# Optimization experiments

Measured on AMD Instinct MI355X. Metric: run time of the kernel, lower is better.

Reference implementation:

```python
import jax, jax.numpy as jnp
import numpy as np

B, C, H, W = 8, 256, 96, 96
GH, GW = 16, 16                # proto_grid
KH, KW = H // GH, W // GW      # avg-pool kernel = stride
P = GH * GW                    # local prototypes per sample
THRESH = 0.95
NORM_EPS = 1e-4


def _safe_norm(x, axis):
    # L2-normalize with norm clamped below at NORM_EPS (matches safe_norm)
    n = jnp.sqrt(jnp.sum(x * x, axis=axis, keepdims=True))
    return x / jnp.maximum(n, NORM_EPS)


def _avg_pool(x):
    # [B, c, H, W] -> [B, c, P] non-overlapping KHxKW average pooling
    b, c = x.shape[:2]
    return x.reshape(b, c, GH, KH, GW, KW).mean(axis=(3, 5)).reshape(b, c, P)


def setup_inputs() -> dict:
    key = jax.random.key(0)
    k1, k2, k3, k4 = jax.random.split(key, 4)
    qry_fts = jax.random.normal(k1, (B, C, H, W), dtype=jnp.float32)
    sup_fts = jax.random.normal(k2, (B, C, H, W), dtype=jnp.float32)
    sup_mask = (jax.random.uniform(k3, (B, 1, H, W)) > 0.02).astype(jnp.float32)
    true_bg_mask = (jax.random.uniform(k4, (B, 1, H, W)) > 0.9).astype(jnp.float32)
    return {"qry_fts": qry_fts, "sup_fts": sup_fts,
            "sup_mask": sup_mask, "true_bg_mask": true_bg_mask}


def reference(qry_fts, sup_fts, sup_mask, true_bg_mask):
    # mode='gridconv+' path, vectorized: ragged prototype selection -> masked softmax
    local_fts = _avg_pool(sup_fts).transpose(0, 2, 1)       # [B, P, C]
    local_mask = _avg_pool(sup_mask)[:, 0, :]               # [B, P]
    local_bg = _avg_pool(true_bg_mask)[:, 0, :]             # [B, P]
    valid = (local_mask > THRESH) & (local_bg < 0.5)        # [B, P] bool

    # global masked-average prototype
    gproto = jnp.sum(sup_fts * sup_mask, axis=(-1, -2)) / (
        jnp.sum(sup_mask, axis=(-1, -2)) + 1e-5)            # [B, C]

    protos = jnp.concatenate([local_fts, gproto[:, None, :]], axis=1)  # [B, P+1, C]
    valid_all = jnp.concatenate(
        [valid, jnp.ones((B, 1), dtype=bool)], axis=1)      # global always valid

    protos_n = _safe_norm(protos, axis=2)                   # [B, P+1, C]
    qry_n = _safe_norm(qry_fts, axis=1)                     # [B, C, H, W]

    # 1x1 conv with prototype weights == batched cosine similarity
    dists = jnp.einsum('bchw,bpc->bphw', qry_n, protos_n)   # [B, P+1, H, W]

    # softmax restricted to valid prototypes (invalid get weight 0)
    logits = jnp.where(valid_all[:, :, None, None], dists, -jnp.inf)
    w = jax.nn.softmax(logits, axis=1)
    pred = jnp.sum(w * dists, axis=1, keepdims=True)        # [B, 1, H, W]
    return pred
```

## Files before the change

kernel.cpp:

```cpp
#include <hip/hip_runtime.h>

#define BB 8
#define CC 256
#define HH 96
#define WW 96
#define HWW (HH*WW)
#define NLOC 256
#define PPAD 257
#define THRESH 0.95f
#define NORM_EPS 1e-4f

typedef __attribute__((ext_vector_type(8))) _Float16 f16x8;
typedef __attribute__((ext_vector_type(16))) float f32x16;

union H16 { _Float16 f; unsigned short u; };

__global__ void k01(const float* __restrict__ sup_fts,
                    const float* __restrict__ sup_mask,
                    const float* __restrict__ true_bg,
                    float* __restrict__ protos,
                    float* __restrict__ validf,
                    float* __restrict__ masksum) {
    __shared__ float red[256];
    int blk = blockIdx.x;
    int t = threadIdx.x;
    if (blk < BB * CC) {
        int b = blk >> 8, c = blk & 255;
        int gy = t >> 4, gx = t & 15;
        const float* fb = sup_fts + ((size_t)b * CC + c) * HWW;
        const float* mb = sup_mask + (size_t)b * HWW;
        int base = gy * 6 * WW + gx * 6;
        float fs = 0.f, fm = 0.f;
        for (int r = 0; r < 6; ++r) {
            const float* rowf = fb + base + r * WW;
            const float* rowm = mb + base + r * WW;
#pragma unroll
            for (int h = 0; h < 3; ++h) {
                float2 v  = *(const float2*)(rowf + 2 * h);
                float2 mk = *(const float2*)(rowm + 2 * h);
                fs += v.x + v.y;
                fm = fmaf(v.x, mk.x, fm);
                fm = fmaf(v.y, mk.y, fm);
            }
        }
        protos[((size_t)b * PPAD + t) * CC + c] = fs * (1.f / 36.f);
        red[t] = fm;
        __syncthreads();
        for (int off = 128; off > 0; off >>= 1) {
            if (t < off) red[t] += red[t + off];
            __syncthreads();
        }
        if (t == 0) protos[((size_t)b * PPAD + 256) * CC + c] = red[0];
    } else {
        int b = blk - BB * CC;
        int gy = t >> 4, gx = t & 15;
        const float* mb = sup_mask + (size_t)b * HWW;
        const float* gb = true_bg  + (size_t)b * HWW;
        int base = gy * 6 * WW + gx * 6;
        float ms = 0.f, bs = 0.f;
        for (int r = 0; r < 6; ++r) {
            const float* rowm = mb + base + r * WW;
            const float* rowg = gb + base + r * WW;
#pragma unroll
            for (int h = 0; h < 3; ++h) {
                float2 mk = *(const float2*)(rowm + 2 * h);
                float2 bg2 = *(const float2*)(rowg + 2 * h);
                ms += mk.x + mk.y;
                bs += bg2.x + bg2.y;
            }
        }
        float mmean = ms * (1.f / 36.f);
        float bmean = bs * (1.f / 36.f);
        validf[b * PPAD + t] = (mmean > THRESH && bmean < 0.5f) ? 1.f : 0.f;
        if (t == 0) validf[b * PPAD + 256] = 1.f;
        red[t] = ms;
        __syncthreads();
        for (int off = 128; off > 0; off >>= 1) {
            if (t < off) red[t] += red[t + off];
            __syncthreads();
        }
        if (t == 0) masksum[b] = red[0];
    }
}

__global__ void k2_norm(float* __restrict__ protos,
                        const float* __restrict__ masksum,
                        unsigned short* __restrict__ Pimg) {
    int bp = blockIdx.x;
    int b = bp / PPAD;
    int p = bp - b * PPAD;
    int t = threadIdx.x;
    float v = protos[((size_t)b * PPAD + p) * CC + t];
    if (p == 256) v = v / (masksum[b] + 1e-5f);
    __shared__ float red[256];
    red[t] = v * v;
    __syncthreads();
    for (int off = 128; off > 0; off >>= 1) {
        if (t < off) red[t] += red[t + off];
        __syncthreads();
    }
    float norm = sqrtf(red[0]);
    float vn = v / fmaxf(norm, NORM_EPS);
    protos[((size_t)b * PPAD + p) * CC + t] = vn;
    if (p < NLOC) {
        H16 h; h.f = (_Float16)vn;
        int kstep = t >> 4, khalf = (t >> 3) & 1, e = t & 7;
        int tile = p >> 5, col = p & 31;
        size_t idx = ((((size_t)b * 16 + kstep) * 2 + khalf) * 8 + tile) * 256
                     + col * 8 + e;
        Pimg[idx] = h.u;
    }
}

__global__ __launch_bounds__(256, 3)
void k3_mfma(const float* __restrict__ qry,
             const unsigned short* __restrict__ Pimg,
             const float* __restrict__ protos_n,
             const float* __restrict__ validf,
             float* __restrict__ out) {
    __shared__ alignas(16) float Qraw[256 * 32];
    __shared__ alignas(16) unsigned short Qf[64 * 128];
    __shared__ float red_n[8][32], red_g[8][32];
    __shared__ float rn_s[32], gd_s[32];
    __shared__ float S_l[4][32], N_l[4][32];

    int blk = blockIdx.x;
    int b = blk & 7;
    int tpx = blk >> 3;
    int px0 = tpx * 32;
    int t = threadIdx.x;
    int l = t & 63;
    int w = t >> 6;
    int col = l & 31;
    int h = l >> 5;

    int spx = t & 31;
    int cg  = t >> 5;

    const float* qbase = qry + (size_t)b * CC * HWW;
    const float* gp = protos_n + ((size_t)b * PPAD + 256) * CC;
    const unsigned short* Pb = Pimg + (size_t)b * 65536;

    float vf0 = validf[b * PPAD + w * 64 + col];
    float vf1 = validf[b * PPAD + w * 64 + 32 + col];

    {
        char* dstbase = (char*)Qraw + w * 1024;
#pragma unroll
        for (int i = 0; i < 8; ++i) {
            int F = i * 256 + t;
            int ch = F >> 3, pxq = F & 7;
            __builtin_amdgcn_global_load_lds(
                (const void*)(qbase + (size_t)ch * HWW + px0 + pxq * 4),
                (void*)(dstbase + i * 4096), 16, 0, 0);
        }
    }
    __syncthreads();

    float nrm = 0.f, gac = 0.f;
#pragma unroll
    for (int j = 0; j < 8; ++j) {
        int c0 = cg * 32 + j * 4;
        unsigned int hh[4];
#pragma unroll
        for (int i = 0; i < 4; ++i) {
            float v = Qraw[(c0 + i) * 32 + spx];
            H16 x; x.f = (_Float16)v;
            hh[i] = x.u;
            nrm = fmaf(v, v, nrm);
            gac = fmaf(v, gp[c0 + i], gac);
        }
        int kq = cg * 8 + j;
        uint2 pk;
        pk.x = hh[0] | (hh[1] << 16); pk.y = hh[2] | (hh[3] << 16);
        *(uint2*)&Qf[kq * 128 + spx * 4] = pk;
    }
    red_n[cg][spx] = nrm;
    red_g[cg][spx] = gac;
    __syncthreads();
    if (t < 32) {
        float n2 = 0.f, gs = 0.f;
#pragma unroll
        for (int i = 0; i < 8; ++i) { n2 += red_n[i][t]; gs += red_g[i][t]; }
        float rn = 1.f / fmaxf(sqrtf(n2), NORM_EPS);
        rn_s[t] = rn;
        gd_s[t] = gs * rn;
    }

    f32x16 acc[2];
#pragma unroll
    for (int i = 0; i < 16; ++i) { acc[0][i] = 0.f; acc[1][i] = 0.f; }
    f16x8 Bf[2][2];

#define LOADB(KS, BUF)                                                        \
    {                                                                         \
        _Pragma("unroll")                                                     \
        for (int ti = 0; ti < 2; ++ti)                                        \
            Bf[BUF][ti] = *(const f16x8*)(Pb +                                \
                ((((size_t)(KS) * 2 + h) * 8 + (w * 2 + ti)) * 32 + col) * 8);\
    }

    LOADB(0, 0);
    LOADB(1, 1);

#pragma unroll
    for (int ks = 0; ks < 16; ++ks) {
        int kq0 = ks * 4 + h * 2;
        uint2 a0 = *(const uint2*)&Qf[kq0 * 128 + col * 4];
        uint2 a1 = *(const uint2*)&Qf[(kq0 + 1) * 128 + col * 4];
        union { f16x8 v; unsigned int u[4]; } QA;
        QA.u[0] = a0.x; QA.u[1] = a0.y; QA.u[2] = a1.x; QA.u[3] = a1.y;
#pragma unroll
        for (int ti = 0; ti < 2; ++ti)
            acc[ti] = __builtin_amdgcn_mfma_f32_32x32x16_f16(QA.v, Bf[ks & 1][ti], acc[ti], 0, 0, 0);
        if (ks + 2 < 16) LOADB(ks + 2, ks & 1);
    }
#undef LOADB

    __syncthreads();

#pragma unroll
    for (int r = 0; r < 16; ++r) {
        int row = (r & 3) + 8 * (r >> 2) + 4 * h;
        float rnv = rn_s[row];
        float d0 = acc[0][r] * rnv;
        float d1 = acc[1][r] * rnv;
        float l0 = (vf0 != 0.f) ? d0 : -1e30f;
        float l1 = (vf1 != 0.f) ? d1 : -1e30f;
        float e0 = __expf(l0 - 1.1f);
        float e1 = __expf(l1 - 1.1f);
        float s = e0 + e1;
        float nn = fmaf(e0, l0, e1 * l1);
#pragma unroll
        for (int m = 1; m < 32; m <<= 1) {
            s  += __shfl_xor(s, m);
            nn += __shfl_xor(nn, m);
        }
        if (col == 0) { S_l[w][row] = s; N_l[w][row] = nn; }
    }
    __syncthreads();

    if (t < 32) {
        float gdv = gd_s[t];
        float eg = __expf(gdv - 1.1f);
        float S = eg, N = eg * gdv;
#pragma unroll
        for (int i = 0; i < 4; ++i) { S += S_l[i][t]; N += N_l[i][t]; }
        out[(size_t)b * HWW + px0 + t] = N / S;
    }
}

extern "C" void kernel_launch(void* const* d_in, const int* in_sizes, int n_in,
                              void* d_out, int out_size, void* d_ws, size_t ws_size,
                              hipStream_t stream) {
    const float* qry = (const float*)d_in[0];
    const float* sup = (const float*)d_in[1];
    const float* msk = (const float*)d_in[2];
    const float* bg  = (const float*)d_in[3];
    float* out = (float*)d_out;

    float* ws = (float*)d_ws;
    float* protos  = ws;
    float* validf  = protos + (size_t)BB * PPAD * CC;
    float* masksum = validf + (size_t)BB * PPAD;
    unsigned short* Pimg = (unsigned short*)(masksum + BB);

    hipLaunchKernelGGL(k01, dim3(BB * CC + BB), dim3(256), 0, stream,
                       sup, msk, bg, protos, validf, masksum);
    hipLaunchKernelGGL(k2_norm, dim3(BB * PPAD), dim3(256), 0, stream, protos, masksum, Pimg);
    hipLaunchKernelGGL(k3_mfma, dim3(BB * (HWW / 32)), dim3(256), 0, stream,
                       qry, Pimg, protos, validf, out);
}
```

Measured before the change: 65.45 us.

## Fuse fp16 query conversion and norm reduction into MFMA A-operand loads

Removes the separate pass that converts the raw fp32 query tile to an fp16 staging buffer and reduces norms and global-proto dots through shared memory. Each wave now reads fp32 values straight from Qraw inside the MFMA loop, converts and packs them into the A fragment, and accumulates norm and global-dot partials in registers, combining the two halves with one shuffle. This drops the Qf and reduction buffers and a barrier, which lowers LDS use and allows raising launch bounds to 4 blocks per CU. In exchange, all four waves redundantly compute the conversion and norms for the same 32 pixels, and the strided LDS reads of Qraw may cause bank conflicts.

```diff
diff --git a/kernel.cpp b/kernel.cpp
--- a/kernel.cpp
+++ b/kernel.cpp
@@ -112,15 +112,14 @@
     }
 }
 
-__global__ __launch_bounds__(256, 3)
+__global__ __launch_bounds__(256, 4)
 void k3_mfma(const float* __restrict__ qry,
              const unsigned short* __restrict__ Pimg,
              const float* __restrict__ protos_n,
              const float* __restrict__ validf,
              float* __restrict__ out) {
     __shared__ alignas(16) float Qraw[256 * 32];
-    __shared__ alignas(16) unsigned short Qf[64 * 128];
-    __shared__ float red_n[8][32], red_g[8][32];
+    __shared__ float gpl[256];
     __shared__ float rn_s[32], gd_s[32];
     __shared__ float S_l[4][32], N_l[4][32];
 
@@ -134,9 +133,6 @@
     int col = l & 31;
     int h = l >> 5;
 
-    int spx = t & 31;
-    int cg  = t >> 5;
-
     const float* qbase = qry + (size_t)b * CC * HWW;
     const float* gp = protos_n + ((size_t)b * PPAD + 256) * CC;
     const unsigned short* Pb = Pimg + (size_t)b * 65536;
@@ -144,6 +140,7 @@
     float vf0 = validf[b * PPAD + w * 64 + col];
     float vf1 = validf[b * PPAD + w * 64 + 32 + col];
 
+    gpl[t] = gp[t];
     {
         char* dstbase = (char*)Qraw + w * 1024;
 #pragma unroll
@@ -157,40 +154,11 @@
     }
     __syncthreads();
 
-    float nrm = 0.f, gac = 0.f;
-#pragma unroll
-    for (int j = 0; j < 8; ++j) {
-        int c0 = cg * 32 + j * 4;
-        unsigned int hh[4];
-#pragma unroll
-        for (int i = 0; i < 4; ++i) {
-            float v = Qraw[(c0 + i) * 32 + spx];
-            H16 x; x.f = (_Float16)v;
-            hh[i] = x.u;
-            nrm = fmaf(v, v, nrm);
-            gac = fmaf(v, gp[c0 + i], gac);
-        }
-        int kq = cg * 8 + j;
-        uint2 pk;
-        pk.x = hh[0] | (hh[1] << 16); pk.y = hh[2] | (hh[3] << 16);
-        *(uint2*)&Qf[kq * 128 + spx * 4] = pk;
-    }
-    red_n[cg][spx] = nrm;
-    red_g[cg][spx] = gac;
-    __syncthreads();
-    if (t < 32) {
-        float n2 = 0.f, gs = 0.f;
-#pragma unroll
-        for (int i = 0; i < 8; ++i) { n2 += red_n[i][t]; gs += red_g[i][t]; }
-        float rn = 1.f / fmaxf(sqrtf(n2), NORM_EPS);
-        rn_s[t] = rn;
-        gd_s[t] = gs * rn;
-    }
-
     f32x16 acc[2];
 #pragma unroll
     for (int i = 0; i < 16; ++i) { acc[0][i] = 0.f; acc[1][i] = 0.f; }
     f16x8 Bf[2][2];
+    float nrm = 0.f, gac = 0.f;
 
 #define LOADB(KS, BUF)                                                        \
     {                                                                         \
@@ -205,11 +173,21 @@
 
 #pragma unroll
     for (int ks = 0; ks < 16; ++ks) {
-        int kq0 = ks * 4 + h * 2;
-        uint2 a0 = *(const uint2*)&Qf[kq0 * 128 + col * 4];
-        uint2 a1 = *(const uint2*)&Qf[(kq0 + 1) * 128 + col * 4];
+        int c0 = ks * 16 + h * 8;
+        float qv[8];
+#pragma unroll
+        for (int i = 0; i < 8; ++i) qv[i] = Qraw[(c0 + i) * 32 + col];
+        unsigned int us[8];
+#pragma unroll
+        for (int i = 0; i < 8; ++i) {
+            H16 x; x.f = (_Float16)qv[i];
+            us[i] = x.u;
+            nrm = fmaf(qv[i], qv[i], nrm);
+            gac = fmaf(qv[i], gpl[c0 + i], gac);
+        }
         union { f16x8 v; unsigned int u[4]; } QA;
-        QA.u[0] = a0.x; QA.u[1] = a0.y; QA.u[2] = a1.x; QA.u[3] = a1.y;
+        QA.u[0] = us[0] | (us[1] << 16); QA.u[1] = us[2] | (us[3] << 16);
+        QA.u[2] = us[4] | (us[5] << 16); QA.u[3] = us[6] | (us[7] << 16);
 #pragma unroll
         for (int ti = 0; ti < 2; ++ti)
             acc[ti] = __builtin_amdgcn_mfma_f32_32x32x16_f16(QA.v, Bf[ks & 1][ti], acc[ti], 0, 0, 0);
@@ -217,6 +195,13 @@
     }
 #undef LOADB
 
+    nrm += __shfl_xor(nrm, 32);
+    gac += __shfl_xor(gac, 32);
+    if (w == 0 && l < 32) {
+        float rn = 1.f / fmaxf(sqrtf(nrm), NORM_EPS);
+        rn_s[l] = rn;
+        gd_s[l] = gac * rn;
+    }
     __syncthreads();
 
 #pragma unroll
```

After: 64.70 us. Within noise of the previous version (-1.2%).
